# Optimization experiments

Hardware: AMD Instinct MI355X
Metric: run time of the kernel (lower is better)

The kernel has to match this reference:

```python
import jax, jax.numpy as jnp
import numpy as np

N_NODES = 100000
N_EDGES = 800000
N_IN = 256
N_H = 128


def setup_inputs() -> dict:
    key = jax.random.key(0)
    ks = jax.random.split(key, 8)
    x_1 = jax.random.normal(ks[0], (1, N_NODES, N_IN), dtype=jnp.float32)
    x_2 = jax.random.normal(ks[1], (1, N_NODES, N_IN), dtype=jnp.float32)
    edge_index = jax.random.randint(ks[2], (2, N_EDGES), 0, N_NODES, dtype=jnp.int32)
    edge_weight = jax.random.uniform(ks[3], (N_EDGES,), dtype=jnp.float32)
    # xavier-uniform-ish init for fc weight (stored as [in, out])
    lim = float(np.sqrt(6.0 / (N_IN + N_H)))
    W_gcn = jax.random.uniform(ks[4], (N_IN, N_H), minval=-lim, maxval=lim, dtype=jnp.float32)
    gcn_bias = jnp.zeros((N_H,), dtype=jnp.float32)
    prelu_a = jnp.full((1,), 0.25, dtype=jnp.float32)  # PReLU default slope
    lim2 = float(np.sqrt(1.0 / N_H))
    lin_W = jax.random.uniform(ks[5], (N_H, N_H), minval=-lim2, maxval=lim2, dtype=jnp.float32)
    lin_b = jax.random.uniform(ks[6], (N_H,), minval=-lim2, maxval=lim2, dtype=jnp.float32)
    return {
        "x_1": x_1, "x_2": x_2, "edge_index": edge_index, "edge_weight": edge_weight,
        "W_gcn": W_gcn, "gcn_bias": gcn_bias, "prelu_a": prelu_a,
        "lin_W": lin_W, "lin_b": lin_b,
    }


def _prelu(x, a):
    return jnp.where(x >= 0, x, a * x)


def _gcn(feat, edge_index, edge_weight, W, b, a, n_nodes):
    # feat: [1, N, n_in] -> h: [N, n_h]
    h = jnp.squeeze(feat, 0) @ W
    row, col = edge_index[0], edge_index[1]
    # spmm: out[i] = sum_{e: row_e = i} w_e * h[col_e]
    msg = edge_weight[:, None] * h[col]            # [E, n_h]
    agg = jax.ops.segment_sum(msg, row, num_segments=n_nodes)  # [N, n_h]
    return _prelu(agg + b, a)                      # [N, n_h]


def reference(x_1, x_2, edge_index, edge_weight, W_gcn, gcn_bias, prelu_a, lin_W, lin_b):
    n = x_1.shape[1]
    h_1 = _gcn(x_1, edge_index, edge_weight, W_gcn, gcn_bias, prelu_a, n)
    h_2 = _gcn(x_2, edge_index, edge_weight, W_gcn, gcn_bias, prelu_a, n)
    z_1 = (h_1 @ lin_W + lin_b).sum(1)   # [N]
    z_2 = (h_2 @ lin_W + lin_b).sum(1)   # [N]
    return jnp.concatenate((z_1, z_2), 0)  # [2N]
```

## Files before the change

kernel.cpp:

```cpp
#include <hip/hip_runtime.h>

#define N_NODES 100000
#define N_EDGES 800000
#define N_IN    256
#define N_H     128
#define M_TOT   (2 * N_NODES)

typedef __bf16 bfx8 __attribute__((ext_vector_type(8)));
typedef unsigned short u16x8 __attribute__((ext_vector_type(8)));
typedef float fx4 __attribute__((ext_vector_type(4)));

__device__ inline unsigned short f2bf(float f) {
    union { float f; unsigned u; } v; v.f = f;
    return (unsigned short)((v.u + 0x7FFF + ((v.u >> 16) & 1)) >> 16);
}
__device__ inline float bf2f(unsigned short s) {
    union { unsigned u; float f; } v; v.u = ((unsigned)s) << 16;
    return v.f;
}

#define WT_S 264
#define NGB  1563
#define NSB  1563

__global__ __launch_bounds__(512, 2) void gemm_scatter_kernel(
        const float* __restrict__ x1, const float* __restrict__ x2,
        const unsigned short* __restrict__ wT,
        unsigned short* __restrict__ hb,
        const int* __restrict__ ei, const float* __restrict__ ew,
        int* __restrict__ cursor, int2* __restrict__ edata) {
    const int t = threadIdx.x;
    if (blockIdx.x >= NGB) {
        int e = (blockIdx.x - NGB) * 512 + t;
        if (e < N_EDGES) {
            int row = ei[e];
            int pos = atomicAdd(cursor + row, 1);
            edata[pos] = make_int2(ei[N_EDGES + e] * N_H, __float_as_int(ew[e]));
        }
        return;
    }
    __shared__ unsigned short wl[N_H * WT_S];
#pragma unroll
    for (int i = 0; i < 8; ++i) {
        int f  = t + i * 512;
        int n  = f >> 5;
        int kp = (f & 31) * 8;
        *(u16x8*)(wl + n * WT_S + kp) = *(const u16x8*)(wT + n * N_IN + kp);
    }
    __syncthreads();

    const int wave = t >> 6, lane = t & 63;
    const int quad = lane >> 4, l16 = lane & 15;
    const int mw = blockIdx.x * 128 + wave * 16;
    if (mw >= M_TOT) return;
    const float* x = (mw < N_NODES) ? x1 : x2;
    const int mrow = (mw < N_NODES) ? mw : mw - N_NODES;

    fx4 acc[8];
#pragma unroll
    for (int c = 0; c < 8; ++c) acc[c] = (fx4){0.f, 0.f, 0.f, 0.f};

    const float* xrow = x + (size_t)(mrow + l16) * N_IN;
#pragma unroll
    for (int kk = 0; kk < N_IN; kk += 32) {
        float4 a0 = *(const float4*)(xrow + kk + quad * 8);
        float4 a1 = *(const float4*)(xrow + kk + quad * 8 + 4);
        u16x8 au;
        au[0] = f2bf(a0.x); au[1] = f2bf(a0.y); au[2] = f2bf(a0.z); au[3] = f2bf(a0.w);
        au[4] = f2bf(a1.x); au[5] = f2bf(a1.y); au[6] = f2bf(a1.z); au[7] = f2bf(a1.w);
        bfx8 af = __builtin_bit_cast(bfx8, au);
#pragma unroll
        for (int c = 0; c < 8; ++c) {
            bfx8 bf = *(const bfx8*)(wl + (size_t)(c * 16 + l16) * WT_S + kk + quad * 8);
            acc[c] = __builtin_amdgcn_mfma_f32_16x16x32_bf16(af, bf, acc[c], 0, 0, 0);
        }
    }
#pragma unroll
    for (int c = 0; c < 8; ++c)
#pragma unroll
        for (int r = 0; r < 4; ++r)
            hb[(size_t)(mw + quad * 4 + r) * N_H + c * 16 + l16] = f2bf(acc[c][r]);
}

#define HIST_BLKS 3125
__global__ __launch_bounds__(256) void prep_kernel(const int* __restrict__ ei,
                                                   int* __restrict__ deg,
                                                   const float* __restrict__ W,
                                                   unsigned short* __restrict__ wT,
                                                   const float* __restrict__ linW,
                                                   const float* __restrict__ linb,
                                                   float* __restrict__ wsum) {
    const int t = threadIdx.x;
    if (blockIdx.x < HIST_BLKS) {
        int e = blockIdx.x * 256 + t;
        if (e < N_EDGES) atomicAdd(deg + ei[e], 1);
    } else if (blockIdx.x < HIST_BLKS + 32) {
        int kb = (blockIdx.x - HIST_BLKS) * 8;
#pragma unroll
        for (int p = 0; p < 4; ++p) {
            int idx = p * 256 + t;
            int k = kb + (idx >> 7), n = idx & 127;
            wT[(size_t)n * N_IN + k] = f2bf(W[(size_t)k * N_H + n]);
        }
    } else {
        int j = t;
        if (j < N_H) {
            float s = 0.f;
            for (int o = 0; o < N_H; ++o) s += linW[j * N_H + o];
            wsum[j] = s;
        }
        if (j == N_H) {
            float s = 0.f;
            for (int o = 0; o < N_H; ++o) s += linb[o];
            wsum[N_H] = s;
        }
    }
}

__global__ __launch_bounds__(256) void scan1_kernel(const int* __restrict__ deg,
                                                    int* __restrict__ part,
                                                    int* __restrict__ bsum) {
    __shared__ int s[256];
    int g = blockIdx.x * 256 + threadIdx.x;
    int v = (g < N_NODES) ? deg[g] : 0;
    s[threadIdx.x] = v;
    __syncthreads();
#pragma unroll
    for (int off = 1; off < 256; off <<= 1) {
        int t = (threadIdx.x >= off) ? s[threadIdx.x - off] : 0;
        __syncthreads();
        s[threadIdx.x] += t;
        __syncthreads();
    }
    if (g < N_NODES) part[g] = s[threadIdx.x] - v;
    if (threadIdx.x == 255) bsum[blockIdx.x] = s[255];
}

#define NBLK_SCAN 391
__global__ void scan2_kernel(int* __restrict__ bsum) {
    __shared__ int s[512];
    int v = (threadIdx.x < NBLK_SCAN) ? bsum[threadIdx.x] : 0;
    s[threadIdx.x] = v;
    __syncthreads();
#pragma unroll
    for (int off = 1; off < 512; off <<= 1) {
        int t = (threadIdx.x >= off) ? s[threadIdx.x - off] : 0;
        __syncthreads();
        s[threadIdx.x] += t;
        __syncthreads();
    }
    if (threadIdx.x < NBLK_SCAN) bsum[threadIdx.x] = s[threadIdx.x] - v;
}

__global__ __launch_bounds__(256) void scan3_kernel(const int* __restrict__ part,
                                                    const int* __restrict__ bsum,
                                                    int* __restrict__ off,
                                                    int* __restrict__ cursor) {
    int g = blockIdx.x * 256 + threadIdx.x;
    if (g < N_NODES) {
        int o = part[g] + bsum[blockIdx.x];
        off[g] = o;
        cursor[g] = o;
    }
    if (g == 0) off[N_NODES] = N_EDGES;
}

__global__ __launch_bounds__(256) void gcn_seg_kernel(const int* __restrict__ off,
                                                      const int2* __restrict__ edata,
                                                      const unsigned short* __restrict__ hb,
                                                      const float* __restrict__ gcn_bias,
                                                      const float* __restrict__ prelu_a,
                                                      const float* __restrict__ wsum,
                                                      float* __restrict__ zout) {
    const int wave = threadIdx.x >> 6, lane = threadIdx.x & 63;
    const int node = blockIdx.x * 4 + wave;
    const unsigned short* h1 = hb;
    const unsigned short* h2 = hb + (size_t)N_NODES * N_H;
    const int s = __builtin_amdgcn_readfirstlane(off[node]);
    const int e = __builtin_amdgcn_readfirstlane(off[node + 1]);
    const int l2 = lane * 2;
    float a0 = 0.f, a1 = 0.f;
    float b0 = 0.f, b1 = 0.f;
    int i = s;
    for (; i + 1 < e; i += 2) {
        int2 E0 = edata[i], E1 = edata[i + 1];
        float w0 = __int_as_float(E0.y), w1 = __int_as_float(E1.y);
        ushort2 p10 = *(const ushort2*)(h1 + E0.x + l2);
        ushort2 p20 = *(const ushort2*)(h2 + E0.x + l2);
        ushort2 p11 = *(const ushort2*)(h1 + E1.x + l2);
        ushort2 p21 = *(const ushort2*)(h2 + E1.x + l2);
        a0 += w0 * bf2f(p10.x) + w1 * bf2f(p11.x);
        a1 += w0 * bf2f(p10.y) + w1 * bf2f(p11.y);
        b0 += w0 * bf2f(p20.x) + w1 * bf2f(p21.x);
        b1 += w0 * bf2f(p20.y) + w1 * bf2f(p21.y);
    }
    if (i < e) {
        int2 E0 = edata[i];
        float w0 = __int_as_float(E0.y);
        ushort2 p10 = *(const ushort2*)(h1 + E0.x + l2);
        ushort2 p20 = *(const ushort2*)(h2 + E0.x + l2);
        a0 += w0 * bf2f(p10.x);
        a1 += w0 * bf2f(p10.y);
        b0 += w0 * bf2f(p20.x);
        b1 += w0 * bf2f(p20.y);
    }
    const float alpha = prelu_a[0];
    const float g0 = gcn_bias[l2], g1 = gcn_bias[l2 + 1];
    const float q0 = wsum[l2],     q1 = wsum[l2 + 1];
    float v0 = a0 + g0, v1 = a1 + g1;
    float u0 = b0 + g0, u1 = b1 + g1;
    v0 = (v0 >= 0.f) ? v0 : alpha * v0;
    v1 = (v1 >= 0.f) ? v1 : alpha * v1;
    u0 = (u0 >= 0.f) ? u0 : alpha * u0;
    u1 = (u1 >= 0.f) ? u1 : alpha * u1;
    float s1 = v0 * q0 + v1 * q1;
    float s2 = u0 * q0 + u1 * q1;
#pragma unroll
    for (int o = 32; o; o >>= 1) {
        s1 += __shfl_down(s1, o, 64);
        s2 += __shfl_down(s2, o, 64);
    }
    if (lane == 0) {
        zout[node]           = s1 + wsum[128];
        zout[node + N_NODES] = s2 + wsum[128];
    }
}

extern "C" void kernel_launch(void* const* d_in, const int* in_sizes, int n_in,
                              void* d_out, int out_size, void* d_ws, size_t ws_size,
                              hipStream_t stream) {
    const float* x1 = (const float*)d_in[0];
    const float* x2 = (const float*)d_in[1];
    const int*   ei = (const int*)d_in[2];
    const float* ew = (const float*)d_in[3];
    const float* Wg = (const float*)d_in[4];
    const float* gb = (const float*)d_in[5];
    const float* pa = (const float*)d_in[6];
    const float* lW = (const float*)d_in[7];
    const float* lb = (const float*)d_in[8];
    float* zout = (float*)d_out;

    unsigned short* hb   = (unsigned short*)d_ws;
    int2*  edata  = (int2*)(hb + (size_t)M_TOT * N_H);
    unsigned short* wT   = (unsigned short*)(edata + N_EDGES);
    int*   deg    = (int*)(wT + N_IN * N_H);
    int*   part   = deg + 100096;
    int*   off    = part + 100096;
    int*   cursor = off + 100096;
    int*   bsum   = cursor + 100096;
    float* wsum   = (float*)(bsum + 512);

    hipMemsetAsync(deg, 0, (size_t)N_NODES * sizeof(int), stream);
    prep_kernel<<<HIST_BLKS + 33, 256, 0, stream>>>(ei, deg, Wg, wT, lW, lb, wsum);
    scan1_kernel<<<NBLK_SCAN, 256, 0, stream>>>(deg, part, bsum);
    scan2_kernel<<<1, 512, 0, stream>>>(bsum);
    scan3_kernel<<<NBLK_SCAN, 256, 0, stream>>>(part, bsum, off, cursor);
    gemm_scatter_kernel<<<NGB + NSB, 512, 0, stream>>>(x1, x2, wT, hb,
                                                       ei, ew, cursor, edata);
    gcn_seg_kernel<<<N_NODES / 4, 256, 0, stream>>>(off, edata, hb, gb, pa, wsum, zout);
}
```

Measured before the change: 395.1 us.

## Pipeline GEMM with async LDS loads, register-held weights, and interleaved h layout

Rewrites the GEMM part as a persistent loop over 16-row tiles. Each tile of x is staged into a swizzled, double-buffered LDS area with async global_load_lds while the previous tile is computed. Weight fragments now live in registers rather than in a large LDS copy, and h1/h2 rows are interleaved per node (stride 256) so the gather in the segment kernel reads both halves from nearby addresses. The scatter blocks are launched first, and the edge-index encoding changes from multiply to shift. The added cost is manual waitcnt and barrier handling, plus extra register pressure from keeping B resident.

New measurement: 387.3 us. 1.02x faster.

```diff
diff --git a/kernel.cpp b/kernel.cpp
--- a/kernel.cpp
+++ b/kernel.cpp
@@ -19,67 +19,98 @@
     return v.f;
 }
 
-#define WT_S 264
-#define NGB  1563
-#define NSB  1563
-
-__global__ __launch_bounds__(512, 2) void gemm_scatter_kernel(
+__device__ inline void async16(const void* g, void* l) {
+    __builtin_amdgcn_global_load_lds((const __attribute__((address_space(1))) void*)g,
+                                     (__attribute__((address_space(3))) void*)l, 16, 0, 0);
+}
+
+#define NT    12500
+#define NTB1  6250
+#define NSB2  3125
+#define NGB2  1024
+
+__global__ __launch_bounds__(256, 4) void gemm_scatter_kernel(
         const float* __restrict__ x1, const float* __restrict__ x2,
         const unsigned short* __restrict__ wT,
         unsigned short* __restrict__ hb,
         const int* __restrict__ ei, const float* __restrict__ ew,
         int* __restrict__ cursor, int2* __restrict__ edata) {
     const int t = threadIdx.x;
-    if (blockIdx.x >= NGB) {
-        int e = (blockIdx.x - NGB) * 512 + t;
-        if (e < N_EDGES) {
-            int row = ei[e];
-            int pos = atomicAdd(cursor + row, 1);
-            edata[pos] = make_int2(ei[N_EDGES + e] * N_H, __float_as_int(ew[e]));
-        }
+    if (blockIdx.x < NSB2) {
+        int e = blockIdx.x * 256 + t;
+        int row = ei[e];
+        int pos = atomicAdd(cursor + row, 1);
+        edata[pos] = make_int2(ei[N_EDGES + e] << 8, __float_as_int(ew[e]));
         return;
     }
-    __shared__ unsigned short wl[N_H * WT_S];
-#pragma unroll
-    for (int i = 0; i < 8; ++i) {
-        int f  = t + i * 512;
-        int n  = f >> 5;
-        int kp = (f & 31) * 8;
-        *(u16x8*)(wl + n * WT_S + kp) = *(const u16x8*)(wT + n * N_IN + kp);
-    }
-    __syncthreads();
-
-    const int wave = t >> 6, lane = t & 63;
-    const int quad = lane >> 4, l16 = lane & 15;
-    const int mw = blockIdx.x * 128 + wave * 16;
-    if (mw >= M_TOT) return;
-    const float* x = (mw < N_NODES) ? x1 : x2;
-    const int mrow = (mw < N_NODES) ? mw : mw - N_NODES;
-
-    fx4 acc[8];
-#pragma unroll
-    for (int c = 0; c < 8; ++c) acc[c] = (fx4){0.f, 0.f, 0.f, 0.f};
-
-    const float* xrow = x + (size_t)(mrow + l16) * N_IN;
-#pragma unroll
-    for (int kk = 0; kk < N_IN; kk += 32) {
-        float4 a0 = *(const float4*)(xrow + kk + quad * 8);
-        float4 a1 = *(const float4*)(xrow + kk + quad * 8 + 4);
-        u16x8 au;
-        au[0] = f2bf(a0.x); au[1] = f2bf(a0.y); au[2] = f2bf(a0.z); au[3] = f2bf(a0.w);
-        au[4] = f2bf(a1.x); au[5] = f2bf(a1.y); au[6] = f2bf(a1.z); au[7] = f2bf(a1.w);
-        bfx8 af = __builtin_bit_cast(bfx8, au);
-#pragma unroll
-        for (int c = 0; c < 8; ++c) {
-            bfx8 bf = *(const bfx8*)(wl + (size_t)(c * 16 + l16) * WT_S + kk + quad * 8);
-            acc[c] = __builtin_amdgcn_mfma_f32_16x16x32_bf16(af, bf, acc[c], 0, 0, 0);
-        }
-    }
-#pragma unroll
-    for (int c = 0; c < 8; ++c)
-#pragma unroll
-        for (int r = 0; r < 4; ++r)
-            hb[(size_t)(mw + quad * 4 + r) * N_H + c * 16 + l16] = f2bf(acc[c][r]);
+    __shared__ __align__(16) float Abuf[2][16][256];
+    const int wv = t >> 6, ln = t & 63;
+    const int quad = ln >> 4, l16 = ln & 15, sw = l16 & 7;
+
+#define STAGE(buf, TT) do {                                                    \
+        int br_ = (TT) >= NTB1;                                                \
+        const float* xs_ = br_ ? x2 : x1;                                      \
+        const float* base_ = xs_ + (size_t)((TT) - br_ * NTB1) * (16 * N_IN);  \
+        _Pragma("unroll")                                                      \
+        for (int i_ = 0; i_ < 4; ++i_) {                                       \
+            int r_ = wv * 4 + i_;                                              \
+            async16(base_ + (size_t)r_ * N_IN + ((ln ^ (r_ & 7)) << 2),        \
+                    &Abuf[(buf)][r_][0]);                                      \
+        }                                                                      \
+    } while (0)
+
+    int T = blockIdx.x - NSB2;
+    STAGE(0, T);
+
+    bfx8 Bf[2][8];
+#pragma unroll
+    for (int c2 = 0; c2 < 2; ++c2)
+#pragma unroll
+        for (int kc = 0; kc < 8; ++kc)
+            Bf[c2][kc] = *(const bfx8*)(wT +
+                (size_t)(wv * 32 + c2 * 16 + l16) * N_IN + kc * 32 + quad * 8);
+
+    int cur = 0;
+    for (; T < NT; T += NGB2) {
+        int Tn = T + NGB2;
+        if (Tn < NT) {
+            STAGE(cur ^ 1, Tn);
+            asm volatile("s_waitcnt vmcnt(4)" ::: "memory");
+        } else {
+            asm volatile("s_waitcnt vmcnt(0)" ::: "memory");
+        }
+        asm volatile("s_barrier" ::: "memory");
+        {
+            int br = T >= NTB1;
+            int node0 = (T - br * NTB1) * 16;
+            fx4 acc0 = {0.f, 0.f, 0.f, 0.f}, acc1 = {0.f, 0.f, 0.f, 0.f};
+            const float* rowp = &Abuf[cur][l16][0];
+#pragma unroll
+            for (int kc = 0; kc < 8; ++kc) {
+                int s0 = kc * 8 + quad * 2;
+                fx4 lo = *(const fx4*)(rowp + (((s0    ) ^ sw) << 2));
+                fx4 hi = *(const fx4*)(rowp + (((s0 + 1) ^ sw) << 2));
+                u16x8 au;
+                au[0] = f2bf(lo[0]); au[1] = f2bf(lo[1]);
+                au[2] = f2bf(lo[2]); au[3] = f2bf(lo[3]);
+                au[4] = f2bf(hi[0]); au[5] = f2bf(hi[1]);
+                au[6] = f2bf(hi[2]); au[7] = f2bf(hi[3]);
+                bfx8 af = __builtin_bit_cast(bfx8, au);
+                acc0 = __builtin_amdgcn_mfma_f32_16x16x32_bf16(af, Bf[0][kc], acc0, 0, 0, 0);
+                acc1 = __builtin_amdgcn_mfma_f32_16x16x32_bf16(af, Bf[1][kc], acc1, 0, 0, 0);
+            }
+            unsigned short* hp = hb + (size_t)node0 * 256 + br * 128 + wv * 32 + l16;
+#pragma unroll
+            for (int r = 0; r < 4; ++r) {
+                size_t off = (size_t)(quad * 4 + r) * 256;
+                hp[off]      = f2bf(acc0[r]);
+                hp[off + 16] = f2bf(acc1[r]);
+            }
+        }
+        asm volatile("s_barrier" ::: "memory");
+        cur ^= 1;
+    }
+#undef STAGE
 }
 
 #define HIST_BLKS 3125
@@ -174,8 +205,6 @@
                                                       float* __restrict__ zout) {
     const int wave = threadIdx.x >> 6, lane = threadIdx.x & 63;
     const int node = blockIdx.x * 4 + wave;
-    const unsigned short* h1 = hb;
-    const unsigned short* h2 = hb + (size_t)N_NODES * N_H;
     const int s = __builtin_amdgcn_readfirstlane(off[node]);
     const int e = __builtin_amdgcn_readfirstlane(off[node + 1]);
     const int l2 = lane * 2;
@@ -185,10 +214,10 @@
     for (; i + 1 < e; i += 2) {
         int2 E0 = edata[i], E1 = edata[i + 1];
         float w0 = __int_as_float(E0.y), w1 = __int_as_float(E1.y);
-        ushort2 p10 = *(const ushort2*)(h1 + E0.x + l2);
-        ushort2 p20 = *(const ushort2*)(h2 + E0.x + l2);
-        ushort2 p11 = *(const ushort2*)(h1 + E1.x + l2);
-        ushort2 p21 = *(const ushort2*)(h2 + E1.x + l2);
+        ushort2 p10 = *(const ushort2*)(hb + E0.x + l2);
+        ushort2 p20 = *(const ushort2*)(hb + E0.x + 128 + l2);
+        ushort2 p11 = *(const ushort2*)(hb + E1.x + l2);
+        ushort2 p21 = *(const ushort2*)(hb + E1.x + 128 + l2);
         a0 += w0 * bf2f(p10.x) + w1 * bf2f(p11.x);
         a1 += w0 * bf2f(p10.y) + w1 * bf2f(p11.y);
         b0 += w0 * bf2f(p20.x) + w1 * bf2f(p21.x);
@@ -197,8 +226,8 @@
     if (i < e) {
         int2 E0 = edata[i];
         float w0 = __int_as_float(E0.y);
-        ushort2 p10 = *(const ushort2*)(h1 + E0.x + l2);
-        ushort2 p20 = *(const ushort2*)(h2 + E0.x + l2);
+        ushort2 p10 = *(const ushort2*)(hb + E0.x + l2);
+        ushort2 p20 = *(const ushort2*)(hb + E0.x + 128 + l2);
         a0 += w0 * bf2f(p10.x);
         a1 += w0 * bf2f(p10.y);
         b0 += w0 * bf2f(p20.x);
@@ -255,7 +284,7 @@
     scan1_kernel<<<NBLK_SCAN, 256, 0, stream>>>(deg, part, bsum);
     scan2_kernel<<<1, 512, 0, stream>>>(bsum);
     scan3_kernel<<<NBLK_SCAN, 256, 0, stream>>>(part, bsum, off, cursor);
-    gemm_scatter_kernel<<<NGB + NSB, 512, 0, stream>>>(x1, x2, wT, hb,
-                                                       ei, ew, cursor, edata);
+    gemm_scatter_kernel<<<NSB2 + NGB2, 256, 0, stream>>>(x1, x2, wT, hb,
+                                                         ei, ew, cursor, edata);
     gcn_seg_kernel<<<N_NODES / 4, 256, 0, stream>>>(off, edata, hb, gb, pa, wsum, zout);
 }
```
